# Performance work log

Measured on AMD Instinct MI355X. Metric: run time of the kernel, lower is better.

The kernel has to match this reference:

```python
import jax, jax.numpy as jnp
import numpy as np

B, C, H, W = 4, 512, 64, 64
DQ = C // 8  # 64


def _conv1x1(x, w, b):
    # x: [B,C,H,W], w: [O,C], b: [O] -> [B,O,H,W]
    return jnp.einsum('bchw,oc->bohw', x, w) + b[None, :, None, None]


def setup_inputs() -> dict:
    key = jax.random.key(0)
    ks = jax.random.split(key, 12)
    s = 0.02  # conv weight init scale
    inp = {
        'x1': jax.random.normal(ks[0], (B, C, H, W), jnp.float32),
        'x2': jax.random.normal(ks[1], (B, C, H, W), jnp.float32),
        'wq1': jax.random.normal(ks[2], (DQ, C), jnp.float32) * s,
        'bq1': jnp.zeros((DQ,), jnp.float32),
        'wk1': jax.random.normal(ks[3], (DQ, C), jnp.float32) * s,
        'bk1': jnp.zeros((DQ,), jnp.float32),
        'wv1': jax.random.normal(ks[4], (C, C), jnp.float32) * s,
        'bv1': jnp.zeros((C,), jnp.float32),
        'wq2': jax.random.normal(ks[5], (DQ, C), jnp.float32) * s,
        'bq2': jnp.zeros((DQ,), jnp.float32),
        'wk2': jax.random.normal(ks[6], (DQ, C), jnp.float32) * s,
        'bk2': jnp.zeros((DQ,), jnp.float32),
        'wv2': jax.random.normal(ks[7], (C, C), jnp.float32) * s,
        'bv2': jnp.zeros((C,), jnp.float32),
        'gamma1': jax.random.normal(ks[8], (1,), jnp.float32) * 0.1,
        'gamma2': jax.random.normal(ks[9], (1,), jnp.float32) * 0.1,
    }
    return inp


def reference(x1, x2, wq1, bq1, wk1, bk1, wv1, bv1,
              wq2, bq2, wk2, bk2, wv2, bv2, gamma1, gamma2):
    b, c, h, w = x1.shape
    n = h * w
    # 1x1-conv projections, flattened to token axis n = h*w
    q1 = _conv1x1(x1, wq1, bq1).reshape(b, -1, n)  # [B,DQ,N]
    k1 = _conv1x1(x1, wk1, bk1).reshape(b, -1, n)  # [B,DQ,N]
    v1 = _conv1x1(x1, wv1, bv1).reshape(b, c, n)   # [B,C,N]
    q2 = _conv1x1(x2, wq2, bq2).reshape(b, -1, n)
    k2 = _conv1x1(x2, wk2, bk2).reshape(b, -1, n)
    v2 = _conv1x1(x2, wv2, bv2).reshape(b, c, n)

    # cross attention 1: queries from x1, keys/values from x2 (no 1/sqrt(d) scaling, per source)
    att1 = jax.nn.softmax(jnp.einsum('bdn,bdm->bnm', q1, k2), axis=-1)  # [B,N,N]
    out1 = jnp.einsum('bcn,bmn->bcm', v2, att1).reshape(b, c, h, w)

    # cross attention 2: queries from x2, keys/values from x1
    att2 = jax.nn.softmax(jnp.einsum('bdn,bdm->bnm', q2, k1), axis=-1)  # [B,N,N]
    out2 = jnp.einsum('bcn,bmn->bcm', v1, att2).reshape(b, c, h, w)

    out1 = x1 + gamma1 * out1
    out2 = x2 + gamma2 * out2
    return out1, out2
```

## Files before the change

kernel.cpp:

```cpp
#include <hip/hip_runtime.h>
#include <hip/hip_bf16.h>

#define NT 4096
#define CD 512
#define DQV 64
#define NB 4

typedef float f32x4 __attribute__((ext_vector_type(4)));
typedef short bf16x8 __attribute__((ext_vector_type(8)));

__device__ __forceinline__ short f2bf(float x){
  union { __hip_bfloat16 b; short s; } u;
  u.b = __float2bfloat16(x);
  return u.s;
}

#define BAR() do { asm volatile("s_waitcnt lgkmcnt(0)" ::: "memory"); \
                   __builtin_amdgcn_s_barrier(); \
                   asm volatile("" ::: "memory"); } while(0)

__global__ void cast_weights(const float* __restrict__ wq1, const float* __restrict__ wk1,
                             const float* __restrict__ wv1, const float* __restrict__ wq2,
                             const float* __restrict__ wk2, const float* __restrict__ wv2,
                             short* __restrict__ out){
  int id = blockIdx.x * 256 + threadIdx.x;
  if (id >= 655360) return;
  float v;
  if (id < 32768)        v = wq1[id];
  else if (id < 65536)   v = wk1[id - 32768];
  else if (id < 327680)  v = wv1[id - 65536];
  else if (id < 360448)  v = wq2[id - 327680];
  else if (id < 393216)  v = wk2[id - 360448];
  else                   v = wv2[id - 393216];
  out[id] = f2bf(v);
}

__global__ void transpose_cast(const float* __restrict__ x1, const float* __restrict__ x2,
                               short* __restrict__ XT1, short* __restrict__ XT2){
  __shared__ short t[64][66];
  int nt = blockIdx.x, ct = blockIdx.y, z = blockIdx.z;
  int b = z & 3, inp = z >> 2;
  const float* xb = (inp ? x2 : x1) + (size_t)b * CD * NT;
  short* xtb = (inp ? XT2 : XT1) + (size_t)b * NT * CD;
  int n0 = nt * 64, c0 = ct * 64;
  int tid = threadIdx.x;
  int nl = tid & 63, cl0 = (tid >> 6) * 2;
#pragma unroll
  for (int cc = 0; cc < 8; ++cc){
    int c = cl0 + cc * 8;
    float v0 = xb[(size_t)(c0 + c) * NT + n0 + nl];
    float v1 = xb[(size_t)(c0 + c + 1) * NT + n0 + nl];
    union { unsigned u; short s[2]; } p;
    p.s[0] = f2bf(v0); p.s[1] = f2bf(v1);
    *(unsigned*)&t[nl][c] = p.u;
  }
  __syncthreads();
  int cl = (tid & 31) * 2, nl0 = tid >> 5;
#pragma unroll
  for (int nn = 0; nn < 8; ++nn){
    int n = nl0 + nn * 8;
    *(unsigned*)&xtb[(size_t)(n0 + n) * CD + c0 + cl] = *(const unsigned*)&t[n][cl];
  }
}

__global__ void proj_qk(const short* __restrict__ XT1, const short* __restrict__ XT2,
                        const short* __restrict__ WB,
                        const float* __restrict__ bq1, const float* __restrict__ bk1,
                        const float* __restrict__ bq2, const float* __restrict__ bk2,
                        short* __restrict__ Q1, short* __restrict__ K1,
                        short* __restrict__ Q2, short* __restrict__ K2){
  int pt = blockIdx.y;
  const short* xt = (pt < 2) ? XT1 : XT2;
  const short* w  = WB + (pt == 0 ? 0 : pt == 1 ? 32768 : pt == 2 ? 327680 : 360448);
  const float* bias = (pt == 0) ? bq1 : (pt == 1) ? bk1 : (pt == 2) ? bq2 : bk2;
  short* out = (pt == 0) ? Q1 : (pt == 1) ? K1 : (pt == 2) ? Q2 : K2;
  int row0 = blockIdx.x * 128;
  int wid = threadIdx.x >> 6, lane = threadIdx.x & 63;
  int lr = lane & 15, lk = (lane >> 4) * 8, lq4 = (lane >> 4) * 4;
  f32x4 acc[2][4] = {};
#pragma unroll 2
  for (int kk = 0; kk < 16; ++kk){
    int k0 = kk * 32 + lk;
    bf16x8 a[2], bb[4];
#pragma unroll
    for (int fr = 0; fr < 2; ++fr)
      a[fr] = *(const bf16x8*)&xt[(size_t)(row0 + wid*32 + fr*16 + lr) * CD + k0];
#pragma unroll
    for (int fc = 0; fc < 4; ++fc)
      bb[fc] = *(const bf16x8*)&w[(size_t)(fc*16 + lr) * CD + k0];
#pragma unroll
    for (int fr = 0; fr < 2; ++fr)
#pragma unroll
      for (int fc = 0; fc < 4; ++fc)
        acc[fr][fc] = __builtin_amdgcn_mfma_f32_16x16x32_bf16(a[fr], bb[fc], acc[fr][fc], 0,0,0);
  }
#pragma unroll
  for (int fr = 0; fr < 2; ++fr)
#pragma unroll
    for (int fc = 0; fc < 4; ++fc){
      int col = fc*16 + lr;
      float bsv = bias[col];
#pragma unroll
      for (int r = 0; r < 4; ++r){
        int row = row0 + wid*32 + fr*16 + lq4 + r;
        out[(size_t)row * DQV + col] = f2bf(acc[fr][fc][r] + bsv);
      }
    }
}

__global__ void proj_v(const short* __restrict__ XT1, const short* __restrict__ XT2,
                       const short* __restrict__ WB,
                       const float* __restrict__ bv1, const float* __restrict__ bv2,
                       short* __restrict__ V1, short* __restrict__ V2){
  int inp = blockIdx.z, b = blockIdx.y;
  int ct = blockIdx.x >> 6, nt = blockIdx.x & 63;
  const short* xt = (inp ? XT2 : XT1) + (size_t)b * NT * CD;
  const short* w  = WB + (inp ? 393216 : 65536);
  const float* bias = inp ? bv2 : bv1;
  short* V = (inp ? V2 : V1) + (size_t)b * CD * NT;
  int c0 = ct * 128, n0 = nt * 64;
  int wid = threadIdx.x >> 6, lane = threadIdx.x & 63;
  int ch = wid >> 1, nh = wid & 1;
  int lr = lane & 15, lk = (lane >> 4) * 8, lq4 = (lane >> 4) * 4;
  f32x4 acc[4][2] = {};
#pragma unroll 2
  for (int kk = 0; kk < 16; ++kk){
    int k0 = kk * 32 + lk;
    bf16x8 a[4], bb[2];
#pragma unroll
    for (int fr = 0; fr < 4; ++fr)
      a[fr] = *(const bf16x8*)&w[(size_t)(c0 + ch*64 + fr*16 + lr) * CD + k0];
#pragma unroll
    for (int fc = 0; fc < 2; ++fc)
      bb[fc] = *(const bf16x8*)&xt[(size_t)(n0 + nh*32 + fc*16 + lr) * CD + k0];
#pragma unroll
    for (int fr = 0; fr < 4; ++fr)
#pragma unroll
      for (int fc = 0; fc < 2; ++fc)
        acc[fr][fc] = __builtin_amdgcn_mfma_f32_16x16x32_bf16(a[fr], bb[fc], acc[fr][fc], 0,0,0);
  }
#pragma unroll
  for (int fr = 0; fr < 4; ++fr)
#pragma unroll
    for (int fc = 0; fc < 2; ++fc)
#pragma unroll
      for (int r = 0; r < 4; ++r){
        int c = c0 + ch*64 + fr*16 + lq4 + r;
        int n = n0 + nh*32 + fc*16 + lr;
        V[(size_t)c * NT + n] = f2bf(acc[fr][fc][r] + bias[c]);
      }
}

__global__ void __launch_bounds__(512, 4) attn_fused(
    const short* __restrict__ Q1, const short* __restrict__ K1, const short* __restrict__ V1,
    const short* __restrict__ Q2, const short* __restrict__ K2, const short* __restrict__ V2,
    const float* __restrict__ x1, const float* __restrict__ x2,
    const float* __restrict__ g1, const float* __restrict__ g2,
    float* __restrict__ out){
  __shared__ float S[64][68];
  __shared__ __align__(16) short P[64][72];
  __shared__ float lrow[64], crow[64];

  int bid = blockIdx.x;
  int pair = bid & 7;
  int rest = bid >> 3;
  int chalf = rest & 1, qb = rest >> 1;
  int b = pair & 3, at = pair >> 2;
  const short* Q = at ? Q2 : Q1;
  const short* K = at ? K1 : K2;
  const short* V = at ? V1 : V2;
  const float* xr = at ? x2 : x1;
  float gamma = at ? g2[0] : g1[0];
  float* outp = out + (size_t)at * NB*CD*NT + (size_t)b * CD*NT;
  const float* xrb = xr + (size_t)b * CD*NT;
  const short* Qb = Q + ((size_t)b*NT + (size_t)qb*64) * DQV;
  const short* Kb = K + (size_t)b*NT*DQV;
  const short* Vb = V + (size_t)b*CD*NT;

  int tid = threadIdx.x, wid = tid >> 6, lane = tid & 63;
  int lr = lane & 15, lk8 = (lane >> 4) * 8, lq4 = (lane >> 4) * 4;

  int ih = wid >> 2, jq = wid & 3;
  bf16x8 qf[2][2];
#pragma unroll
  for (int fr = 0; fr < 2; ++fr)
#pragma unroll
    for (int fk = 0; fk < 2; ++fk)
      qf[fr][fk] = *(const bf16x8*)&Qb[(size_t)(ih*32 + fr*16 + lr) * DQV + fk*32 + lk8];

  f32x4 acc[2][4] = {};
  int c0 = chalf * 256 + wid * 32;
  int si = tid >> 3, sj = (tid & 7) * 8;
  float m_reg = -1e30f, l_reg = 0.f;

#pragma unroll 1
  for (int jt = 0; jt < 64; ++jt){
    int j0 = jt * 64;
    bf16x8 vf[2][2];
#pragma unroll
    for (int cr = 0; cr < 2; ++cr)
#pragma unroll
      for (int kk = 0; kk < 2; ++kk)
        vf[cr][kk] = *(const bf16x8*)&Vb[(size_t)(c0 + cr*16 + lr) * NT + j0 + kk*32 + lk8];
    f32x4 s0 = {}, s1 = {};
#pragma unroll
    for (int fk = 0; fk < 2; ++fk){
      bf16x8 kf = *(const bf16x8*)&Kb[(size_t)(j0 + jq*16 + lr) * DQV + fk*32 + lk8];
      s0 = __builtin_amdgcn_mfma_f32_16x16x32_bf16(qf[0][fk], kf, s0, 0,0,0);
      s1 = __builtin_amdgcn_mfma_f32_16x16x32_bf16(qf[1][fk], kf, s1, 0,0,0);
    }
#pragma unroll
    for (int r = 0; r < 4; ++r){
      S[ih*32 + lq4 + r][jq*16 + lr]      = s0[r];
      S[ih*32 + 16 + lq4 + r][jq*16 + lr] = s1[r];
    }
    BAR();
    {
      f32x4 sa = *(const f32x4*)&S[si][sj];
      f32x4 sb = *(const f32x4*)&S[si][sj + 4];
      float mx = fmaxf(fmaxf(fmaxf(sa[0], sa[1]), fmaxf(sa[2], sa[3])),
                       fmaxf(fmaxf(sb[0], sb[1]), fmaxf(sb[2], sb[3])));
      mx = fmaxf(mx, __shfl_xor(mx, 1));
      mx = fmaxf(mx, __shfl_xor(mx, 2));
      mx = fmaxf(mx, __shfl_xor(mx, 4));
      float mn = fmaxf(m_reg, mx);
      float cf = __expf(m_reg - mn);
      float e0 = __expf(sa[0] - mn), e1 = __expf(sa[1] - mn);
      float e2 = __expf(sa[2] - mn), e3 = __expf(sa[3] - mn);
      float e4 = __expf(sb[0] - mn), e5 = __expf(sb[1] - mn);
      float e6 = __expf(sb[2] - mn), e7 = __expf(sb[3] - mn);
      float sum = ((e0 + e1) + (e2 + e3)) + ((e4 + e5) + (e6 + e7));
      bf16x8 pv;
      pv[0] = f2bf(e0); pv[1] = f2bf(e1); pv[2] = f2bf(e2); pv[3] = f2bf(e3);
      pv[4] = f2bf(e4); pv[5] = f2bf(e5); pv[6] = f2bf(e6); pv[7] = f2bf(e7);
      *(bf16x8*)&P[si][sj] = pv;
      sum += __shfl_xor(sum, 1);
      sum += __shfl_xor(sum, 2);
      sum += __shfl_xor(sum, 4);
      l_reg = l_reg * cf + sum;
      m_reg = mn;
      if ((tid & 7) == 0) crow[si] = cf;
    }
    BAR();
    {
      float cfa[4];
#pragma unroll
      for (int ci = 0; ci < 4; ++ci) cfa[ci] = crow[ci*16 + lr];
      bool ident = (cfa[0] == 1.f) & (cfa[1] == 1.f) & (cfa[2] == 1.f) & (cfa[3] == 1.f);
      if (!__all(ident)){
#pragma unroll
        for (int ci = 0; ci < 4; ++ci){
          float cf = cfa[ci];
#pragma unroll
          for (int cr = 0; cr < 2; ++cr){
            acc[cr][ci][0] *= cf; acc[cr][ci][1] *= cf;
            acc[cr][ci][2] *= cf; acc[cr][ci][3] *= cf;
          }
        }
      }
    }
    __builtin_amdgcn_s_setprio(1);
#pragma unroll
    for (int kk = 0; kk < 2; ++kk){
      bf16x8 pf[4];
#pragma unroll
      for (int ci = 0; ci < 4; ++ci)
        pf[ci] = *(const bf16x8*)&P[ci*16 + lr][kk*32 + lk8];
#pragma unroll
      for (int cr = 0; cr < 2; ++cr)
#pragma unroll
        for (int ci = 0; ci < 4; ++ci)
          acc[cr][ci] = __builtin_amdgcn_mfma_f32_16x16x32_bf16(vf[cr][kk], pf[ci], acc[cr][ci], 0,0,0);
    }
    __builtin_amdgcn_s_setprio(0);
  }
  if ((tid & 7) == 0) lrow[si] = l_reg;
  BAR();
#pragma unroll
  for (int ci = 0; ci < 4; ++ci){
    float linv = 1.f / lrow[ci*16 + lr];
    int ig = qb*64 + ci*16 + lr;
#pragma unroll
    for (int cr = 0; cr < 2; ++cr)
#pragma unroll
      for (int r = 0; r < 4; ++r){
        int c = c0 + cr*16 + lq4 + r;
        size_t idx = (size_t)c * NT + ig;
        outp[idx] = xrb[idx] + gamma * acc[cr][ci][r] * linv;
      }
  }
}

extern "C" void kernel_launch(void* const* d_in, const int* in_sizes, int n_in,
                              void* d_out, int out_size, void* d_ws, size_t ws_size,
                              hipStream_t stream) {
  const float* x1  = (const float*)d_in[0];
  const float* x2  = (const float*)d_in[1];
  const float* wq1 = (const float*)d_in[2];
  const float* bq1 = (const float*)d_in[3];
  const float* wk1 = (const float*)d_in[4];
  const float* bk1 = (const float*)d_in[5];
  const float* wv1 = (const float*)d_in[6];
  const float* bv1 = (const float*)d_in[7];
  const float* wq2 = (const float*)d_in[8];
  const float* bq2 = (const float*)d_in[9];
  const float* wk2 = (const float*)d_in[10];
  const float* bk2 = (const float*)d_in[11];
  const float* wv2 = (const float*)d_in[12];
  const float* bv2 = (const float*)d_in[13];
  const float* g1  = (const float*)d_in[14];
  const float* g2  = (const float*)d_in[15];

  short* XT1 = (short*)d_ws;
  short* XT2 = XT1 + 8388608;
  short* Q1  = XT2 + 8388608;
  short* K1  = Q1 + 1048576;
  short* Q2  = K1 + 1048576;
  short* K2  = Q2 + 1048576;
  short* V1  = K2 + 1048576;
  short* V2  = V1 + 8388608;
  short* WB  = V2 + 8388608;

  cast_weights<<<2560, 256, 0, stream>>>(wq1, wk1, wv1, wq2, wk2, wv2, WB);
  transpose_cast<<<dim3(64, 8, 8), 256, 0, stream>>>(x1, x2, XT1, XT2);
  proj_qk<<<dim3(128, 4), 256, 0, stream>>>(XT1, XT2, WB, bq1, bk1, bq2, bk2, Q1, K1, Q2, K2);
  proj_v<<<dim3(256, 4, 2), 256, 0, stream>>>(XT1, XT2, WB, bv1, bv2, V1, V2);
  attn_fused<<<1024, 512, 0, stream>>>(Q1, K1, V1, Q2, K2, V2, x1, x2, g1, g2, (float*)d_out);
}
```

Measured before the change: 621.3 us.

## Double-buffer score tiles to drop one barrier per iteration and swizzle P

The QK^T scores for the next key tile are now computed during the current iteration's softmax and written into a second S buffer. This removes one of the two block barriers per loop iteration. The P tile is double-buffered too and stored with an XOR column swizzle instead of padding, to avoid LDS bank conflicts on the PV fragment reads. In exchange it uses more LDS and keeps the prefetched K fragments live in registers, which may lower occupancy.

```diff
diff --git a/kernel.cpp b/kernel.cpp
--- a/kernel.cpp
+++ b/kernel.cpp
@@ -157,9 +157,9 @@
     const float* __restrict__ x1, const float* __restrict__ x2,
     const float* __restrict__ g1, const float* __restrict__ g2,
     float* __restrict__ out){
-  __shared__ float S[64][68];
-  __shared__ __align__(16) short P[64][72];
-  __shared__ float lrow[64], crow[64];
+  __shared__ float S[2][64][68];
+  __shared__ __align__(16) short P[2][64][64];
+  __shared__ float lrow[64], crow[2][64];
 
   int bid = blockIdx.x;
   int pair = bid & 7;
@@ -191,10 +191,31 @@
   f32x4 acc[2][4] = {};
   int c0 = chalf * 256 + wid * 32;
   int si = tid >> 3, sj = (tid & 7) * 8;
+  int pcol = sj ^ ((si & 7) * 8);
   float m_reg = -1e30f, l_reg = 0.f;
+
+  {
+    bf16x8 kf[2];
+#pragma unroll
+    for (int fk = 0; fk < 2; ++fk)
+      kf[fk] = *(const bf16x8*)&Kb[(size_t)(jq*16 + lr) * DQV + fk*32 + lk8];
+    f32x4 s0 = {}, s1 = {};
+#pragma unroll
+    for (int fk = 0; fk < 2; ++fk){
+      s0 = __builtin_amdgcn_mfma_f32_16x16x32_bf16(qf[0][fk], kf[fk], s0, 0,0,0);
+      s1 = __builtin_amdgcn_mfma_f32_16x16x32_bf16(qf[1][fk], kf[fk], s1, 0,0,0);
+    }
+#pragma unroll
+    for (int r = 0; r < 4; ++r){
+      S[0][ih*32 + lq4 + r][jq*16 + lr]      = s0[r];
+      S[0][ih*32 + 16 + lq4 + r][jq*16 + lr] = s1[r];
+    }
+  }
+  BAR();
 
 #pragma unroll 1
   for (int jt = 0; jt < 64; ++jt){
+    int buf = jt & 1, nbuf = buf ^ 1;
     int j0 = jt * 64;
     bf16x8 vf[2][2];
 #pragma unroll
@@ -202,22 +223,15 @@
 #pragma unroll
       for (int kk = 0; kk < 2; ++kk)
         vf[cr][kk] = *(const bf16x8*)&Vb[(size_t)(c0 + cr*16 + lr) * NT + j0 + kk*32 + lk8];
-    f32x4 s0 = {}, s1 = {};
-#pragma unroll
-    for (int fk = 0; fk < 2; ++fk){
-      bf16x8 kf = *(const bf16x8*)&Kb[(size_t)(j0 + jq*16 + lr) * DQV + fk*32 + lk8];
-      s0 = __builtin_amdgcn_mfma_f32_16x16x32_bf16(qf[0][fk], kf, s0, 0,0,0);
-      s1 = __builtin_amdgcn_mfma_f32_16x16x32_bf16(qf[1][fk], kf, s1, 0,0,0);
-    }
-#pragma unroll
-    for (int r = 0; r < 4; ++r){
-      S[ih*32 + lq4 + r][jq*16 + lr]      = s0[r];
-      S[ih*32 + 16 + lq4 + r][jq*16 + lr] = s1[r];
-    }
-    BAR();
+    bf16x8 kf[2];
+    if (jt < 63){
+#pragma unroll
+      for (int fk = 0; fk < 2; ++fk)
+        kf[fk] = *(const bf16x8*)&Kb[(size_t)(j0 + 64 + jq*16 + lr) * DQV + fk*32 + lk8];
+    }
     {
-      f32x4 sa = *(const f32x4*)&S[si][sj];
-      f32x4 sb = *(const f32x4*)&S[si][sj + 4];
+      f32x4 sa = *(const f32x4*)&S[buf][si][sj];
+      f32x4 sb = *(const f32x4*)&S[buf][si][sj + 4];
       float mx = fmaxf(fmaxf(fmaxf(sa[0], sa[1]), fmaxf(sa[2], sa[3])),
                        fmaxf(fmaxf(sb[0], sb[1]), fmaxf(sb[2], sb[3])));
       mx = fmaxf(mx, __shfl_xor(mx, 1));
@@ -233,19 +247,32 @@
       bf16x8 pv;
       pv[0] = f2bf(e0); pv[1] = f2bf(e1); pv[2] = f2bf(e2); pv[3] = f2bf(e3);
       pv[4] = f2bf(e4); pv[5] = f2bf(e5); pv[6] = f2bf(e6); pv[7] = f2bf(e7);
-      *(bf16x8*)&P[si][sj] = pv;
+      *(bf16x8*)&P[buf][si][pcol] = pv;
       sum += __shfl_xor(sum, 1);
       sum += __shfl_xor(sum, 2);
       sum += __shfl_xor(sum, 4);
       l_reg = l_reg * cf + sum;
       m_reg = mn;
-      if ((tid & 7) == 0) crow[si] = cf;
+      if ((tid & 7) == 0) crow[buf][si] = cf;
+    }
+    if (jt < 63){
+      f32x4 s0 = {}, s1 = {};
+#pragma unroll
+      for (int fk = 0; fk < 2; ++fk){
+        s0 = __builtin_amdgcn_mfma_f32_16x16x32_bf16(qf[0][fk], kf[fk], s0, 0,0,0);
+        s1 = __builtin_amdgcn_mfma_f32_16x16x32_bf16(qf[1][fk], kf[fk], s1, 0,0,0);
+      }
+#pragma unroll
+      for (int r = 0; r < 4; ++r){
+        S[nbuf][ih*32 + lq4 + r][jq*16 + lr]      = s0[r];
+        S[nbuf][ih*32 + 16 + lq4 + r][jq*16 + lr] = s1[r];
+      }
     }
     BAR();
     {
       float cfa[4];
 #pragma unroll
-      for (int ci = 0; ci < 4; ++ci) cfa[ci] = crow[ci*16 + lr];
+      for (int ci = 0; ci < 4; ++ci) cfa[ci] = crow[buf][ci*16 + lr];
       bool ident = (cfa[0] == 1.f) & (cfa[1] == 1.f) & (cfa[2] == 1.f) & (cfa[3] == 1.f);
       if (!__all(ident)){
 #pragma unroll
@@ -264,8 +291,11 @@
     for (int kk = 0; kk < 2; ++kk){
       bf16x8 pf[4];
 #pragma unroll
-      for (int ci = 0; ci < 4; ++ci)
-        pf[ci] = *(const bf16x8*)&P[ci*16 + lr][kk*32 + lk8];
+      for (int ci = 0; ci < 4; ++ci){
+        int row = ci*16 + lr;
+        int col = (kk*32 + lk8) ^ ((row & 7) * 8);
+        pf[ci] = *(const bf16x8*)&P[buf][row][col];
+      }
 #pragma unroll
       for (int cr = 0; cr < 2; ++cr)
 #pragma unroll
```

Measured after the change: 624.7 us. No clear change (+0.5%).
